# Performance work log

Hardware: AMD Instinct MI355X
Metric: run time of the kernel (lower is better)

## Reference

```python
import math
import jax, jax.numpy as jnp
import numpy as np

B, S, E, H = 4, 2048, 1024, 16
HD = E // H  # 64


def setup_inputs() -> dict:
    key = jax.random.key(0)
    ks = jax.random.split(key, 7)
    scale = 1.0 / math.sqrt(E)
    return {
        "x": jax.random.normal(ks[0], (B, S, E), dtype=jnp.float32),
        "Wq": jax.random.normal(ks[1], (H, HD, E), dtype=jnp.float32) * scale,
        "bq": jax.random.normal(ks[2], (H, HD), dtype=jnp.float32) * 0.01,
        "Wk": jax.random.normal(ks[3], (H, HD, E), dtype=jnp.float32) * scale,
        "bk": jax.random.normal(ks[4], (H, HD), dtype=jnp.float32) * 0.01,
        "Wv": jax.random.normal(ks[5], (H, HD, E), dtype=jnp.float32) * scale,
        "bv": jax.random.normal(ks[6], (H, HD), dtype=jnp.float32) * 0.01,
    }


def reference(x, Wq, bq, Wk, bk, Wv, bv):
    b, s, e = x.shape
    h, hd, _ = Wq.shape
    inv_scale = 1.0 / math.sqrt(hd)
    # per-head linear projections (torch Linear: x @ W^T + b), batched over heads
    q = jnp.einsum("bse,hde->bshd", x, Wq) + bq  # [B,S,H,HD]
    k = jnp.einsum("bse,hde->bshd", x, Wk) + bk
    v = jnp.einsum("bse,hde->bshd", x, Wv) + bv
    # causal mask: -inf above diagonal (added before scaling, as in source;
    # -inf * inv_scale is still -inf so math is identical)
    mask = jnp.triu(jnp.full((s, s), -jnp.inf, dtype=x.dtype), k=1)
    scores = (jnp.einsum("bqhd,bkhd->bhqk", q, k) + mask) * inv_scale  # [B,H,S,S]
    attn = jax.nn.softmax(scores, axis=-1)
    out = jnp.einsum("bhqk,bkhd->bqhd", attn, v)  # [B,S,H,HD]
    # concat over heads in head order == reshape with head-major last dims
    return out.reshape(b, s, h * hd)
```

## Files before the change

### kernel.cpp

```cpp
#include <hip/hip_runtime.h>


typedef __bf16 bf16x8 __attribute__((ext_vector_type(8)));
typedef __bf16 bf16x4 __attribute__((ext_vector_type(4)));
typedef float f32x4 __attribute__((ext_vector_type(4)));
typedef unsigned short us8 __attribute__((ext_vector_type(8)));
typedef unsigned short us4 __attribute__((ext_vector_type(4)));

#define Bb 4
#define Ss 2048
#define Ee 1024
#define Hh 16
#define HD 64

#if __has_builtin(__builtin_amdgcn_exp2f)
#define EXP2(x) __builtin_amdgcn_exp2f(x)
#else
#define EXP2(x) exp2f(x)
#endif

__device__ __forceinline__ unsigned short f2bf(float f) {
  union { float f; unsigned u; } v; v.f = f;
  unsigned u = v.u;
  u += 0x7fffu + ((u >> 16) & 1u);
  return (unsigned short)(u >> 16);
}

__device__ __forceinline__ void gl_lds16(const void* g, void* l) {
  __builtin_amdgcn_global_load_lds((const __attribute__((address_space(1))) void*)g,
                                   (__attribute__((address_space(3))) void*)l, 16, 0, 0);
}

#define DSR(d, a, o) asm volatile("ds_read_b128 %0, %1 offset:" #o : "=v"(d) : "v"(a))

__global__ __launch_bounds__(256) void cvt_all(const float* __restrict__ x,
                                               const float* __restrict__ wq,
                                               const float* __restrict__ wk,
                                               const float* __restrict__ wv,
                                               unsigned short* __restrict__ xb,
                                               unsigned short* __restrict__ wb) {
  int i = blockIdx.x * 256 + threadIdx.x;
  const float* src; unsigned short* dst; int idx;
  if (i < 2097152)      { src = x;  dst = xb;                idx = i; }
  else if (i < 2359296) { src = wq; dst = wb;                idx = i - 2097152; }
  else if (i < 2621440) { src = wk; dst = wb + 1048576;      idx = i - 2359296; }
  else                  { src = wv; dst = wb + 2 * 1048576;  idx = i - 2621440; }
  float4 f = ((const float4*)src)[idx];
  us4 o = { f2bf(f.x), f2bf(f.y), f2bf(f.z), f2bf(f.w) };
  ((us4*)dst)[idx] = o;
}

__global__ __launch_bounds__(512, 2) void qkv_gemm(const unsigned short* __restrict__ xb,
                                                   const unsigned short* __restrict__ wb_all,
                                                   const float* __restrict__ bq,
                                                   const float* __restrict__ bk,
                                                   const float* __restrict__ bv,
                                                   unsigned short* __restrict__ qkv) {
  const int z = blockIdx.z;
  const unsigned short* wb = wb_all + (size_t)z * (Ee * Ee);
  const float* bias = (z == 0) ? bq : (z == 1) ? bk : bv;
  unsigned short* outb = qkv + (size_t)z * (Bb * Ss * Ee);
  const float osc = (z == 0) ? 0.180336880f : 1.0f;

  __shared__ unsigned short SMEM[65536];

  const int t = threadIdx.x;
  const int wave = t >> 6, lane = t & 63, quad = lane >> 4, ln = lane & 15;
  const int wr = wave >> 2, wc = wave & 3;
  const int m0 = blockIdx.x * 256, n0 = blockIdx.y * 256;

  const int r8 = t >> 3;
  const int cs = ((t & 7) ^ (r8 & 7)) * 8;
  const int t8 = t * 8;
  const unsigned short* gA0 = xb + (size_t)(m0 + r8) * Ee + cs;
  const unsigned short* gA1 = gA0 + 128 * Ee;
  const unsigned short* gB0 = wb + (size_t)(n0 + r8) * Ee + cs;
  const unsigned short* gB1 = gB0 + 128 * Ee;

  const int swz0 = ((0 * 4 + quad) ^ (ln & 7)) * 16;
  const int swz1 = ((1 * 4 + quad) ^ (ln & 7)) * 16;
  int aA0 = (wr * 64 + ln) * 128 + swz0;
  int aA1 = (wr * 64 + ln) * 128 + swz1;
  int bA0 = 32768 + (wc * 32 + ln) * 128 + swz0;
  int bA1 = 32768 + (wc * 32 + ln) * 128 + swz1;

  f32x4 acc[2][2][4][2] = {};
  bf16x8 af[4][2], bf0[2][2], bf1[2][2];

  gl_lds16(gA0,           &SMEM[t8]);
  gl_lds16(gA0 + 64 * Ee, &SMEM[t8 + 4096]);
  gl_lds16(gB0,           &SMEM[16384 + t8]);
  gl_lds16(gB0 + 64 * Ee, &SMEM[16384 + t8 + 4096]);
  gl_lds16(gB1,           &SMEM[24576 + t8]);
  gl_lds16(gB1 + 64 * Ee, &SMEM[24576 + t8 + 4096]);
  gl_lds16(gA1,           &SMEM[8192 + t8]);
  gl_lds16(gA1 + 64 * Ee, &SMEM[8192 + t8 + 4096]);

#pragma unroll 1
  for (int kt = 0; kt < 15; ++kt) {
    const int sbuf = ((kt & 1) << 15) ^ 32768;
    const int co = (kt + 1) * 64;

    asm volatile("s_waitcnt vmcnt(4)" ::: "memory");
    asm volatile("s_barrier" ::: "memory");
    DSR(af[0][0], aA0, 0);    DSR(af[1][0], aA0, 2048);
    DSR(af[2][0], aA0, 4096); DSR(af[3][0], aA0, 6144);
    DSR(af[0][1], aA1, 0);    DSR(af[1][1], aA1, 2048);
    DSR(af[2][1], aA1, 4096); DSR(af[3][1], aA1, 6144);
    DSR(bf0[0][0], bA0, 0);   DSR(bf0[1][0], bA0, 2048);
    DSR(bf0[0][1], bA1, 0);   DSR(bf0[1][1], bA1, 2048);
    gl_lds16(gA0 + co,           &SMEM[sbuf + t8]);
    gl_lds16(gA0 + co + 64 * Ee, &SMEM[sbuf + t8 + 4096]);
    asm volatile("s_barrier" ::: "memory");
    asm volatile("s_waitcnt lgkmcnt(0)" ::: "memory");
    __builtin_amdgcn_sched_barrier(0);
    __builtin_amdgcn_s_setprio(1);
#pragma unroll
    for (int kk = 0; kk < 2; ++kk)
#pragma unroll
      for (int i = 0; i < 4; ++i)
#pragma unroll
        for (int j = 0; j < 2; ++j)
          acc[0][0][i][j] = __builtin_amdgcn_mfma_f32_16x16x32_bf16(af[i][kk], bf0[j][kk], acc[0][0][i][j], 0, 0, 0);
    __builtin_amdgcn_s_setprio(0);
    __builtin_amdgcn_sched_barrier(0);

    asm volatile("s_waitcnt vmcnt(4)" ::: "memory");
    asm volatile("s_barrier" ::: "memory");
    DSR(bf1[0][0], bA0, 16384); DSR(bf1[1][0], bA0, 18432);
    DSR(bf1[0][1], bA1, 16384); DSR(bf1[1][1], bA1, 18432);
    gl_lds16(gB0 + co,           &SMEM[sbuf + 16384 + t8]);
    gl_lds16(gB0 + co + 64 * Ee, &SMEM[sbuf + 16384 + t8 + 4096]);
    asm volatile("s_barrier" ::: "memory");
    asm volatile("s_waitcnt lgkmcnt(0)" ::: "memory");
    __builtin_amdgcn_sched_barrier(0);
    __builtin_amdgcn_s_setprio(1);
#pragma unroll
    for (int kk = 0; kk < 2; ++kk)
#pragma unroll
      for (int i = 0; i < 4; ++i)
#pragma unroll
        for (int j = 0; j < 2; ++j)
          acc[0][1][i][j] = __builtin_amdgcn_mfma_f32_16x16x32_bf16(af[i][kk], bf1[j][kk], acc[0][1][i][j], 0, 0, 0);
    __builtin_amdgcn_s_setprio(0);
    __builtin_amdgcn_sched_barrier(0);

    asm volatile("s_waitcnt vmcnt(4)" ::: "memory");
    asm volatile("s_barrier" ::: "memory");
    DSR(af[0][0], aA0, 16384); DSR(af[1][0], aA0, 18432);
    DSR(af[2][0], aA0, 20480); DSR(af[3][0], aA0, 22528);
    DSR(af[0][1], aA1, 16384); DSR(af[1][1], aA1, 18432);
    DSR(af[2][1], aA1, 20480); DSR(af[3][1], aA1, 22528);
    gl_lds16(gB1 + co,           &SMEM[sbuf + 24576 + t8]);
    gl_lds16(gB1 + co + 64 * Ee, &SMEM[sbuf + 24576 + t8 + 4096]);
    asm volatile("s_barrier" ::: "memory");
    asm volatile("s_waitcnt lgkmcnt(0)" ::: "memory");
    __builtin_amdgcn_sched_barrier(0);
    __builtin_amdgcn_s_setprio(1);
#pragma unroll
    for (int kk = 0; kk < 2; ++kk)
#pragma unroll
      for (int i = 0; i < 4; ++i)
#pragma unroll
        for (int j = 0; j < 2; ++j)
          acc[1][0][i][j] = __builtin_amdgcn_mfma_f32_16x16x32_bf16(af[i][kk], bf0[j][kk], acc[1][0][i][j], 0, 0, 0);
    __builtin_amdgcn_s_setprio(0);
    __builtin_amdgcn_sched_barrier(0);

    asm volatile("s_barrier" ::: "memory");
    gl_lds16(gA1 + co,           &SMEM[sbuf + 8192 + t8]);
    gl_lds16(gA1 + co + 64 * Ee, &SMEM[sbuf + 8192 + t8 + 4096]);
    asm volatile("s_barrier" ::: "memory");
    __builtin_amdgcn_sched_barrier(0);
    __builtin_amdgcn_s_setprio(1);
#pragma unroll
    for (int kk = 0; kk < 2; ++kk)
#pragma unroll
      for (int i = 0; i < 4; ++i)
#pragma unroll
        for (int j = 0; j < 2; ++j)
          acc[1][1][i][j] = __builtin_amdgcn_mfma_f32_16x16x32_bf16(af[i][kk], bf1[j][kk], acc[1][1][i][j], 0, 0, 0);
    __builtin_amdgcn_s_setprio(0);
    __builtin_amdgcn_sched_barrier(0);

    aA0 ^= 65536; aA1 ^= 65536; bA0 ^= 65536; bA1 ^= 65536;
  }

  {
    asm volatile("s_waitcnt vmcnt(0)" ::: "memory");
    asm volatile("s_barrier" ::: "memory");
    DSR(af[0][0], aA0, 0);    DSR(af[1][0], aA0, 2048);
    DSR(af[2][0], aA0, 4096); DSR(af[3][0], aA0, 6144);
    DSR(af[0][1], aA1, 0);    DSR(af[1][1], aA1, 2048);
    DSR(af[2][1], aA1, 4096); DSR(af[3][1], aA1, 6144);
    DSR(bf0[0][0], bA0, 0);   DSR(bf0[1][0], bA0, 2048);
    DSR(bf0[0][1], bA1, 0);   DSR(bf0[1][1], bA1, 2048);
    DSR(bf1[0][0], bA0, 16384); DSR(bf1[1][0], bA0, 18432);
    DSR(bf1[0][1], bA1, 16384); DSR(bf1[1][1], bA1, 18432);
    asm volatile("s_waitcnt lgkmcnt(0)" ::: "memory");
    __builtin_amdgcn_sched_barrier(0);
#pragma unroll
    for (int kk = 0; kk < 2; ++kk)
#pragma unroll
      for (int i = 0; i < 4; ++i)
#pragma unroll
        for (int j = 0; j < 2; ++j) {
          acc[0][0][i][j] = __builtin_amdgcn_mfma_f32_16x16x32_bf16(af[i][kk], bf0[j][kk], acc[0][0][i][j], 0, 0, 0);
          acc[0][1][i][j] = __builtin_amdgcn_mfma_f32_16x16x32_bf16(af[i][kk], bf1[j][kk], acc[0][1][i][j], 0, 0, 0);
        }
    __builtin_amdgcn_sched_barrier(0);
    DSR(af[0][0], aA0, 16384); DSR(af[1][0], aA0, 18432);
    DSR(af[2][0], aA0, 20480); DSR(af[3][0], aA0, 22528);
    DSR(af[0][1], aA1, 16384); DSR(af[1][1], aA1, 18432);
    DSR(af[2][1], aA1, 20480); DSR(af[3][1], aA1, 22528);
    asm volatile("s_waitcnt lgkmcnt(0)" ::: "memory");
    __builtin_amdgcn_sched_barrier(0);
#pragma unroll
    for (int kk = 0; kk < 2; ++kk)
#pragma unroll
      for (int i = 0; i < 4; ++i)
#pragma unroll
        for (int j = 0; j < 2; ++j) {
          acc[1][0][i][j] = __builtin_amdgcn_mfma_f32_16x16x32_bf16(af[i][kk], bf0[j][kk], acc[1][0][i][j], 0, 0, 0);
          acc[1][1][i][j] = __builtin_amdgcn_mfma_f32_16x16x32_bf16(af[i][kk], bf1[j][kk], acc[1][1][i][j], 0, 0, 0);
        }
    __builtin_amdgcn_sched_barrier(0);
  }

  float biasj[2][2];
#pragma unroll
  for (int qb = 0; qb < 2; ++qb)
#pragma unroll
    for (int j = 0; j < 2; ++j)
      biasj[qb][j] = bias[n0 + qb * 128 + wc * 32 + j * 16 + ln];

  if (z != 2) {
#pragma unroll
    for (int qa = 0; qa < 2; ++qa)
#pragma unroll
      for (int qb = 0; qb < 2; ++qb)
#pragma unroll
        for (int i = 0; i < 4; ++i)
#pragma unroll
          for (int j = 0; j < 2; ++j)
#pragma unroll
            for (int r = 0; r < 4; ++r) {
              int m = m0 + qa * 128 + wr * 64 + i * 16 + quad * 4 + r;
              int n = n0 + qb * 128 + wc * 32 + j * 16 + ln;
              int b_ = m >> 11, s = m & 2047;
              int h = n >> 6, d = n & 63;
              outb[(((size_t)b_ * Hh + h) * Ss + s) * HD + d] =
                  f2bf((acc[qa][qb][i][j][r] + biasj[qb][j]) * osc);
            }
  } else {
    for (int qa = 0; qa < 2; ++qa) {
      __syncthreads();
#pragma unroll
      for (int qb = 0; qb < 2; ++qb)
#pragma unroll
        for (int i = 0; i < 4; ++i)
#pragma unroll
          for (int j = 0; j < 2; ++j)
#pragma unroll
            for (int r = 0; r < 4; ++r) {
              int nc = qb * 128 + wc * 32 + j * 16 + ln;
              int mr = wr * 64 + i * 16 + quad * 4 + r;
              SMEM[nc * 136 + mr] = f2bf(acc[qa][qb][i][j][r] + biasj[qb][j]);
            }
      __syncthreads();
      int nr = t >> 1, mh = t & 1;
      int n = n0 + nr, h = n >> 6, d = n & 63;
      int b_ = m0 >> 11;
      int s0 = (m0 & 2047) + qa * 128 + mh * 64;
#pragma unroll
      for (int q = 0; q < 8; ++q) {
        us8 vdat = *(const us8*)&SMEM[nr * 136 + mh * 64 + q * 8];
        *(us8*)&outb[(((size_t)b_ * Hh + h) * HD + d) * Ss + s0 + q * 8] = vdat;
      }
    }
  }
}

__global__ __launch_bounds__(256) void flash_attn(const unsigned short* __restrict__ qkv,
                                                  float* __restrict__ out) {
  const int id = blockIdx.x;
  const int bh = id & 63;
  const int p = id >> 6;
  const int b_ = bh >> 4, h = bh & 15;

  const unsigned short* qb  = qkv + (size_t)bh * (Ss * HD);
  const unsigned short* kb  = qkv + (size_t)(64 + bh) * (Ss * HD);
  const unsigned short* vtb = qkv + (size_t)(128 + bh) * (Ss * HD);

  __shared__ __bf16 Ks[4096];
  __shared__ __bf16 Vt[4096];
  __shared__ __bf16 Ps[4][2][16][72];

  const int t = threadIdx.x;
  const int wave = t >> 6, lane = t & 63, quad = lane >> 4, ln = lane & 15;

  const int r0 = t >> 3;
  const int c0 = ((t & 7) ^ (r0 & 7)) * 8;
  const int koff0 = r0 * HD + c0;
  const int koff1 = koff0 + 32 * HD;
  const int voff0 = r0 * Ss + c0;
  const int voff1 = voff0 + 32 * Ss;
  __bf16* Kl0 = &Ks[t * 8];  __bf16* Kl1 = &Ks[2048 + t * 8];
  __bf16* Vl0 = &Vt[t * 8];  __bf16* Vl1 = &Vt[2048 + t * 8];

  int kslot[4][2];
#pragma unroll
  for (int g = 0; g < 4; ++g)
#pragma unroll
    for (int ks = 0; ks < 2; ++ks)
      kslot[g][ks] = ((g * 16 + ln) * 8 + ((ks * 4 + quad) ^ (ln & 7))) * 8;

  bf16x8 onef;
#pragma unroll
  for (int j = 0; j < 8; ++j) onef[j] = (__bf16)1.0f;

  const int qtps[2] = { 15 - p, p };

  for (int ph = 0; ph < 2; ++ph) {
    const int qtp = qtps[ph];
    const int q0 = qtp * 128;

    bf16x8 qf[2][2];
#pragma unroll
    for (int u = 0; u < 2; ++u)
#pragma unroll
      for (int ks = 0; ks < 2; ++ks)
        qf[u][ks] = *(const bf16x8*)(qb + (size_t)(q0 + u * 64 + wave * 16 + ln) * HD +
                                     ks * 32 + quad * 8);

    f32x4 o[2][4] = {};
    f32x4 l4[2] = {};
    const int ktmax = 2 * qtp + 1;

    for (int kt = 0; kt <= ktmax; ++kt) {
      const unsigned short* kbt = kb + kt * (64 * HD);
      const unsigned short* vbt = vtb + kt * 64;
      __syncthreads();
      gl_lds16(kbt + koff0, Kl0);
      gl_lds16(kbt + koff1, Kl1);
      gl_lds16(vbt + voff0, Vl0);
      gl_lds16(vbt + voff1, Vl1);
      __syncthreads();

#pragma unroll
      for (int u = 0; u < 2; ++u) {
        if (u == 0 && kt == ktmax) continue;
        const int qrow = q0 + u * 64 + wave * 16 + ln;

        f32x4 s_acc[4] = {};
#pragma unroll
        for (int g = 0; g < 4; ++g)
#pragma unroll
          for (int ks = 0; ks < 2; ++ks) {
            bf16x8 kf = *(const bf16x8*)&Ks[kslot[g][ks]];
            s_acc[g] = __builtin_amdgcn_mfma_f32_16x16x32_bf16(kf, qf[u][ks], s_acc[g], 0, 0, 0);
          }

        if (kt == 2 * qtp + u) {
          const int k0 = kt * 64;
#pragma unroll
          for (int g = 0; g < 4; ++g)
#pragma unroll
            for (int r = 0; r < 4; ++r) {
              int kcol = k0 + g * 16 + quad * 4 + r;
              if (kcol > qrow) s_acc[g][r] = -__builtin_inff();
            }
        }

#pragma unroll
        for (int g = 0; g < 4; ++g) {
          bf16x4 pk = { (__bf16)EXP2(s_acc[g][0]), (__bf16)EXP2(s_acc[g][1]),
                        (__bf16)EXP2(s_acc[g][2]), (__bf16)EXP2(s_acc[g][3]) };
          *(bf16x4*)&Ps[wave][u][ln][g * 16 + quad * 4] = pk;
        }
        bf16x8 pf[2];
#pragma unroll
        for (int ks = 0; ks < 2; ++ks)
          pf[ks] = *(const bf16x8*)&Ps[wave][u][ln][ks * 32 + quad * 8];

        l4[u] = __builtin_amdgcn_mfma_f32_16x16x32_bf16(pf[0], onef, l4[u], 0, 0, 0);
        l4[u] = __builtin_amdgcn_mfma_f32_16x16x32_bf16(pf[1], onef, l4[u], 0, 0, 0);

#pragma unroll
        for (int g = 0; g < 4; ++g)
#pragma unroll
          for (int ks = 0; ks < 2; ++ks) {
            bf16x8 vf = *(const bf16x8*)&Vt[kslot[g][ks]];
            o[u][g] = __builtin_amdgcn_mfma_f32_16x16x32_bf16(pf[ks], vf, o[u][g], 0, 0, 0);
          }
      }
    }

#pragma unroll
    for (int u = 0; u < 2; ++u) {
      float linv[4];
#pragma unroll
      for (int r = 0; r < 4; ++r) linv[r] = 1.0f / l4[u][r];
#pragma unroll
      for (int g = 0; g < 4; ++g)
#pragma unroll
        for (int r = 0; r < 4; ++r) {
          int orow = q0 + u * 64 + wave * 16 + quad * 4 + r;
          out[((size_t)b_ * Ss + orow) * Ee + h * HD + g * 16 + ln] = o[u][g][r] * linv[r];
        }
    }
    __syncthreads();
  }
}

extern "C" void kernel_launch(void* const* d_in, const int* in_sizes, int n_in,
                              void* d_out, int out_size, void* d_ws, size_t ws_size,
                              hipStream_t stream) {
  const float* x  = (const float*)d_in[0];
  const float* Wq = (const float*)d_in[1];
  const float* bq = (const float*)d_in[2];
  const float* Wk = (const float*)d_in[3];
  const float* bk = (const float*)d_in[4];
  const float* Wv = (const float*)d_in[5];
  const float* bv = (const float*)d_in[6];
  float* out = (float*)d_out;

  unsigned short* ws  = (unsigned short*)d_ws;
  unsigned short* xb  = ws;
  unsigned short* wb  = ws + 8388608;
  unsigned short* qkv = ws + 8388608 + 3 * 1048576;

  cvt_all<<<11264, 256, 0, stream>>>(x, Wq, Wk, Wv, xb, wb);
  qkv_gemm<<<dim3(32, 4, 3), 512, 0, stream>>>(xb, wb, bq, bk, bv, qkv);
  flash_attn<<<512, 256, 0, stream>>>(qkv, out);
}
```

Measured before the change: 217.8 us.

## Share K/V tiles across both paired query tiles with 128-wide key blocks

The attention kernel now processes both paired query tiles (15-p and p) in one pass over the key/value sequence, so K and V tiles loaded into LDS are reused by both instead of being reloaded in two phases. Key tiles grow from 64 to 128 keys per load, which halves the number of barrier pairs, and launch bounds request two blocks per CU. The cost is more live accumulators (o and l for four query subtiles), which raises register pressure, and twice the LDS per block.

```diff
diff --git a/kernel.cpp b/kernel.cpp
--- a/kernel.cpp
+++ b/kernel.cpp
@@ -281,8 +281,8 @@
   }
 }
 
-__global__ __launch_bounds__(256) void flash_attn(const unsigned short* __restrict__ qkv,
-                                                  float* __restrict__ out) {
+__global__ __launch_bounds__(256, 2) void flash_attn(const unsigned short* __restrict__ qkv,
+                                                     float* __restrict__ out) {
   const int id = blockIdx.x;
   const int bh = id & 63;
   const int p = id >> 6;
@@ -292,125 +292,129 @@
   const unsigned short* kb  = qkv + (size_t)(64 + bh) * (Ss * HD);
   const unsigned short* vtb = qkv + (size_t)(128 + bh) * (Ss * HD);
 
-  __shared__ __bf16 Ks[4096];
-  __shared__ __bf16 Vt[4096];
-  __shared__ __bf16 Ps[4][2][16][72];
+  __shared__ __bf16 Ks[8192];
+  __shared__ __bf16 Vt[8192];
+  __shared__ __bf16 Ps[4][16][72];
 
   const int t = threadIdx.x;
   const int wave = t >> 6, lane = t & 63, quad = lane >> 4, ln = lane & 15;
 
-  const int r0 = t >> 3;
-  const int c0 = ((t & 7) ^ (r0 & 7)) * 8;
-  const int koff0 = r0 * HD + c0;
-  const int koff1 = koff0 + 32 * HD;
-  const int voff0 = r0 * Ss + c0;
-  const int voff1 = voff0 + 32 * Ss;
-  __bf16* Kl0 = &Ks[t * 8];  __bf16* Kl1 = &Ks[2048 + t * 8];
-  __bf16* Vl0 = &Vt[t * 8];  __bf16* Vl1 = &Vt[2048 + t * 8];
-
-  int kslot[4][2];
-#pragma unroll
-  for (int g = 0; g < 4; ++g)
-#pragma unroll
-    for (int ks = 0; ks < 2; ++ks)
-      kslot[g][ks] = ((g * 16 + ln) * 8 + ((ks * 4 + quad) ^ (ln & 7))) * 8;
+  const int rk = t >> 3;
+  const int ck = ((t & 7) ^ (rk & 7)) * 8;
+  const int rv = t >> 4;
+  const int cv = ((t & 15) ^ (rv & 7)) * 8;
+  const int t8 = t * 8;
+
+  const int qts[2] = { 15 - p, p };
+  const int KTB = qts[0] + 1;
+
+  bf16x8 qf[2][2][2];
+#pragma unroll
+  for (int qt = 0; qt < 2; ++qt)
+#pragma unroll
+    for (int u = 0; u < 2; ++u)
+#pragma unroll
+      for (int ks = 0; ks < 2; ++ks)
+        qf[qt][u][ks] = *(const bf16x8*)(qb + (size_t)(qts[qt] * 128 + u * 64 + wave * 16 + ln) * HD +
+                                         ks * 32 + quad * 8);
 
   bf16x8 onef;
 #pragma unroll
   for (int j = 0; j < 8; ++j) onef[j] = (__bf16)1.0f;
 
-  const int qtps[2] = { 15 - p, p };
-
-  for (int ph = 0; ph < 2; ++ph) {
-    const int qtp = qtps[ph];
-    const int q0 = qtp * 128;
-
-    bf16x8 qf[2][2];
-#pragma unroll
-    for (int u = 0; u < 2; ++u)
-#pragma unroll
-      for (int ks = 0; ks < 2; ++ks)
-        qf[u][ks] = *(const bf16x8*)(qb + (size_t)(q0 + u * 64 + wave * 16 + ln) * HD +
-                                     ks * 32 + quad * 8);
-
-    f32x4 o[2][4] = {};
-    f32x4 l4[2] = {};
-    const int ktmax = 2 * qtp + 1;
-
-    for (int kt = 0; kt <= ktmax; ++kt) {
-      const unsigned short* kbt = kb + kt * (64 * HD);
-      const unsigned short* vbt = vtb + kt * 64;
-      __syncthreads();
-      gl_lds16(kbt + koff0, Kl0);
-      gl_lds16(kbt + koff1, Kl1);
-      gl_lds16(vbt + voff0, Vl0);
-      gl_lds16(vbt + voff1, Vl1);
-      __syncthreads();
-
-#pragma unroll
-      for (int u = 0; u < 2; ++u) {
-        if (u == 0 && kt == ktmax) continue;
-        const int qrow = q0 + u * 64 + wave * 16 + ln;
-
-        f32x4 s_acc[4] = {};
-#pragma unroll
-        for (int g = 0; g < 4; ++g)
-#pragma unroll
-          for (int ks = 0; ks < 2; ++ks) {
-            bf16x8 kf = *(const bf16x8*)&Ks[kslot[g][ks]];
-            s_acc[g] = __builtin_amdgcn_mfma_f32_16x16x32_bf16(kf, qf[u][ks], s_acc[g], 0, 0, 0);
+  f32x4 o[2][2][4] = {};
+  f32x4 l4[2][2] = {};
+
+#pragma unroll 1
+  for (int kt = 0; kt < KTB; ++kt) {
+    const unsigned short* kbt = kb + (size_t)kt * (128 * HD);
+    const unsigned short* vbt = vtb + kt * 128;
+    __syncthreads();
+    gl_lds16(kbt + rk * HD + ck,        &Ks[t8]);
+    gl_lds16(kbt + (rk + 32) * HD + ck, &Ks[t8 + 2048]);
+    gl_lds16(kbt + (rk + 64) * HD + ck, &Ks[t8 + 4096]);
+    gl_lds16(kbt + (rk + 96) * HD + ck, &Ks[t8 + 6144]);
+    gl_lds16(vbt + rv * Ss + cv,        &Vt[t8]);
+    gl_lds16(vbt + (rv + 16) * Ss + cv, &Vt[t8 + 2048]);
+    gl_lds16(vbt + (rv + 32) * Ss + cv, &Vt[t8 + 4096]);
+    gl_lds16(vbt + (rv + 48) * Ss + cv, &Vt[t8 + 6144]);
+    __syncthreads();
+
+#pragma unroll
+    for (int h2 = 0; h2 < 2; ++h2) {
+      const int kb64 = kt * 2 + h2;
+#pragma unroll
+      for (int qt = 0; qt < 2; ++qt) {
+        const int qtp = qts[qt];
+#pragma unroll
+        for (int u = 0; u < 2; ++u) {
+          const int su = 2 * qtp + u;
+          if (kb64 > su) continue;
+          const int qrow = qtp * 128 + u * 64 + wave * 16 + ln;
+
+          f32x4 s_acc[4] = {};
+#pragma unroll
+          for (int g = 0; g < 4; ++g)
+#pragma unroll
+            for (int ks = 0; ks < 2; ++ks) {
+              bf16x8 kf = *(const bf16x8*)&Ks[(h2 * 64 + g * 16 + ln) * 64 +
+                                              (((ks * 4 + quad) ^ (ln & 7)) * 8)];
+              s_acc[g] = __builtin_amdgcn_mfma_f32_16x16x32_bf16(kf, qf[qt][u][ks], s_acc[g], 0, 0, 0);
+            }
+
+          if (kb64 == su) {
+            const int k0 = kb64 * 64;
+#pragma unroll
+            for (int g = 0; g < 4; ++g)
+#pragma unroll
+              for (int r = 0; r < 4; ++r) {
+                int kcol = k0 + g * 16 + quad * 4 + r;
+                if (kcol > qrow) s_acc[g][r] = -__builtin_inff();
+              }
           }
 
-        if (kt == 2 * qtp + u) {
-          const int k0 = kt * 64;
+#pragma unroll
+          for (int g = 0; g < 4; ++g) {
+            bf16x4 pk = { (__bf16)EXP2(s_acc[g][0]), (__bf16)EXP2(s_acc[g][1]),
+                          (__bf16)EXP2(s_acc[g][2]), (__bf16)EXP2(s_acc[g][3]) };
+            *(bf16x4*)&Ps[wave][ln][g * 16 + quad * 4] = pk;
+          }
+          bf16x8 pf[2];
+#pragma unroll
+          for (int ks = 0; ks < 2; ++ks)
+            pf[ks] = *(const bf16x8*)&Ps[wave][ln][ks * 32 + quad * 8];
+
+          l4[qt][u] = __builtin_amdgcn_mfma_f32_16x16x32_bf16(pf[0], onef, l4[qt][u], 0, 0, 0);
+          l4[qt][u] = __builtin_amdgcn_mfma_f32_16x16x32_bf16(pf[1], onef, l4[qt][u], 0, 0, 0);
+
 #pragma unroll
           for (int g = 0; g < 4; ++g)
 #pragma unroll
-            for (int r = 0; r < 4; ++r) {
-              int kcol = k0 + g * 16 + quad * 4 + r;
-              if (kcol > qrow) s_acc[g][r] = -__builtin_inff();
+            for (int ks = 0; ks < 2; ++ks) {
+              bf16x8 vf = *(const bf16x8*)&Vt[(g * 16 + ln) * 128 +
+                                              (((h2 * 8 + ks * 4 + quad) ^ (ln & 7)) * 8)];
+              o[qt][u][g] = __builtin_amdgcn_mfma_f32_16x16x32_bf16(pf[ks], vf, o[qt][u][g], 0, 0, 0);
             }
         }
-
-#pragma unroll
-        for (int g = 0; g < 4; ++g) {
-          bf16x4 pk = { (__bf16)EXP2(s_acc[g][0]), (__bf16)EXP2(s_acc[g][1]),
-                        (__bf16)EXP2(s_acc[g][2]), (__bf16)EXP2(s_acc[g][3]) };
-          *(bf16x4*)&Ps[wave][u][ln][g * 16 + quad * 4] = pk;
-        }
-        bf16x8 pf[2];
-#pragma unroll
-        for (int ks = 0; ks < 2; ++ks)
-          pf[ks] = *(const bf16x8*)&Ps[wave][u][ln][ks * 32 + quad * 8];
-
-        l4[u] = __builtin_amdgcn_mfma_f32_16x16x32_bf16(pf[0], onef, l4[u], 0, 0, 0);
-        l4[u] = __builtin_amdgcn_mfma_f32_16x16x32_bf16(pf[1], onef, l4[u], 0, 0, 0);
-
-#pragma unroll
-        for (int g = 0; g < 4; ++g)
-#pragma unroll
-          for (int ks = 0; ks < 2; ++ks) {
-            bf16x8 vf = *(const bf16x8*)&Vt[kslot[g][ks]];
-            o[u][g] = __builtin_amdgcn_mfma_f32_16x16x32_bf16(pf[ks], vf, o[u][g], 0, 0, 0);
-          }
       }
     }
-
+  }
+
+#pragma unroll
+  for (int qt = 0; qt < 2; ++qt)
 #pragma unroll
     for (int u = 0; u < 2; ++u) {
       float linv[4];
 #pragma unroll
-      for (int r = 0; r < 4; ++r) linv[r] = 1.0f / l4[u][r];
+      for (int r = 0; r < 4; ++r) linv[r] = 1.0f / l4[qt][u][r];
 #pragma unroll
       for (int g = 0; g < 4; ++g)
 #pragma unroll
         for (int r = 0; r < 4; ++r) {
-          int orow = q0 + u * 64 + wave * 16 + quad * 4 + r;
-          out[((size_t)b_ * Ss + orow) * Ee + h * HD + g * 16 + ln] = o[u][g][r] * linv[r];
+          int orow = qts[qt] * 128 + u * 64 + wave * 16 + quad * 4 + r;
+          out[((size_t)b_ * Ss + orow) * Ee + h * HD + g * 16 + ln] = o[qt][u][g][r] * linv[r];
         }
     }
-    __syncthreads();
-  }
 }
 
 extern "C" void kernel_launch(void* const* d_in, const int* in_sizes, int n_in,
```

Result: faster. 213.5 us (-2.0%).
